# Kernel optimization log

Measured on AMD Instinct MI355X. Metric: run time of the kernel, lower is better.

The kernel has to match this reference:

```python
import jax, jax.numpy as jnp
import numpy as np

N, E, G = 50000, 800000, 64          # nodes, edges, graphs in batch
IN, H, F = 128, 4, 32                # in_dim, num_heads, out_feats per head
HD = H * F                           # 128 = flattened head dim
HID, OUT = 32, 10                    # hidden_dim, num classes
EPS, SLOPE = 1e-5, 0.2               # BN eps, leaky_relu negative slope


def batchnorm(x, g, b):
    mu = x.mean(0)
    var = x.var(0)  # biased, as torch BN in training mode
    return g * (x - mu) * jax.lax.rsqrt(var + EPS) + b


def gatv2(feat, src, dst, W, fb, attn, ob):
    # shared-weights GATv2: same fc for src and dst
    h = (feat @ W + fb).reshape(-1, H, F)           # [N,H,F]
    el = h[src]                                     # [E,H,F] gather
    er = h[dst]
    e = jnp.einsum('ehf,hf->eh', jax.nn.leaky_relu(el + er, SLOPE), attn)  # [E,H]
    # edge softmax over incoming edges of each dst node
    m = jax.ops.segment_max(e, dst, num_segments=N)
    m = jax.lax.stop_gradient(jnp.where(jnp.isfinite(m), m, 0.0))
    ex = jnp.exp(e - m[dst])
    den = jax.ops.segment_sum(ex, dst, num_segments=N)
    alpha = ex / jnp.where(den > 0, den, 1.0)[dst]  # zero in-degree -> zeros
    out = jax.ops.segment_sum((el * alpha[:, :, None]).reshape(-1, HD), dst,
                              num_segments=N)       # [N,HD]
    return jax.nn.relu(out + ob)                    # conv activation, flattened heads


def _forward(feat, src, dst, seg,
             w0, fb0, a0, ob0, bg0, bb0, lw0, lb0, lg0, lbt0,
             w1, fb1, a1, ob1, bg1, bb1, lw1, lb1, lg1, lbt1,
             w2, fb2, a2, ob2, bg2, bb2, lw2, lb2, lg2, lbt2,
             mw1, mg, mb, mw2):
    layers = [
        (w0, fb0, a0, ob0, bg0, bb0, lw0, lb0, lg0, lbt0),
        (w1, fb1, a1, ob1, bg1, bb1, lw1, lb1, lg1, lbt1),
        (w2, fb2, a2, ob2, bg2, bb2, lw2, lb2, lg2, lbt2),
    ]
    x = feat
    pooled = []
    for (W, fb, a, ob, bg, bb, lw, lb, lg, lbt) in layers:
        x = gatv2(x, src, dst, W, fb, a, ob)        # [N,HD]
        x = batchnorm(x, bg, bb)
        p = jax.ops.segment_sum(x, seg, num_segments=G)  # sum pool -> [G,HD]
        p = jax.nn.relu(p @ lw + lb)                # linear_prediction
        pooled.append(batchnorm(p, lg, lbt))        # [G,HID]
    ph = jnp.concatenate(pooled, axis=-1)           # [G, 3*HID]
    hmid = jax.nn.relu(batchnorm(ph @ mw1, mg, mb)) # MLP layer 1 (no bias)
    logits = hmid @ mw2                             # MLP layer 2 (no bias)
    return jax.nn.log_softmax(logits, axis=-1)      # [G,OUT]


def setup_inputs() -> dict:
    key = jax.random.key(0)
    ks = iter(jax.random.split(key, 64))
    d = {}
    d['feat'] = jax.random.normal(next(ks), (N, IN), dtype=jnp.float32)
    d['src'] = jax.random.randint(next(ks), (E,), 0, N, dtype=jnp.int32)
    d['dst'] = jax.random.randint(next(ks), (E,), 0, N, dtype=jnp.int32)
    d['seg'] = jnp.sort(jax.random.randint(next(ks), (N,), 0, G, dtype=jnp.int32))
    for i in range(3):
        d[f'w{i}'] = jax.random.normal(next(ks), (HD if i else IN, HD)) * 0.05
        d[f'fb{i}'] = jnp.zeros((HD,))
        d[f'a{i}'] = jax.random.normal(next(ks), (H, F)) * 0.05
        d[f'ob{i}'] = jnp.zeros((HD,))
        d[f'bg{i}'] = jnp.ones((HD,))
        d[f'bb{i}'] = jnp.zeros((HD,))
        d[f'lw{i}'] = jax.random.normal(next(ks), (HD, HID)) * 0.05
        d[f'lb{i}'] = jnp.zeros((HID,))
        d[f'lg{i}'] = jnp.ones((HID,))
        d[f'lbt{i}'] = jnp.zeros((HID,))
    d['mw1'] = jax.random.normal(next(ks), (3 * HID, HID)) * 0.05
    d['mg'] = jnp.ones((HID,))
    d['mb'] = jnp.zeros((HID,))
    d['mw2'] = jax.random.normal(next(ks), (HID, OUT)) * 0.05
    return d


def reference(feat, src, dst, seg,
              w0, fb0, a0, ob0, bg0, bb0, lw0, lb0, lg0, lbt0,
              w1, fb1, a1, ob1, bg1, bb1, lw1, lb1, lg1, lbt1,
              w2, fb2, a2, ob2, bg2, bb2, lw2, lb2, lg2, lbt2,
              mw1, mg, mb, mw2):
    return _forward(feat, src, dst, seg,
                    w0, fb0, a0, ob0, bg0, bb0, lw0, lb0, lg0, lbt0,
                    w1, fb1, a1, ob1, bg1, bb1, lw1, lb1, lg1, lbt1,
                    w2, fb2, a2, ob2, bg2, bb2, lw2, lb2, lg2, lbt2,
                    mw1, mg, mb, mw2)
```

## Files before the change

### kernel.cpp

```cpp
#include <hip/hip_runtime.h>
#include <math.h>

#define N_NODES 50000
#define N_EDGES 800000
#define G_GRAPHS 64
#define HDIM 128
#define HID 32
#define NCLS 10
#define BN_EPS 1e-5f
#define SLOPE 0.2f
#define NB_SCAN 196
#define STATS_STRIDE (256 + G_GRAPHS * HDIM)
#define DEFER_THR 8.0f

#define NBUCK 64
#define NPB 782
#define CH 4096
#define NCHUNK 196
#define NGB_GEMM 782
#define CAP_OUT 13824
#define NZ_DWORDS (64 + 3 * STATS_STRIDE + 64)

typedef __attribute__((ext_vector_type(8))) short bf16x8;
typedef __attribute__((ext_vector_type(4))) float f32x4;

__device__ __forceinline__ float lrelu(float x) { return fmaxf(x, SLOPE * x); }

__device__ __forceinline__ unsigned short f2bf(float x) {
    unsigned int u = __float_as_uint(x);
    u = (u + 0x7fffu + ((u >> 16) & 1u)) >> 16;
    return (unsigned short)u;
}
__device__ __forceinline__ unsigned int pk2bf(float lo, float hi) {
    unsigned int r;
    asm("v_cvt_pk_bf16_f32 %0, %1, %2" : "=v"(r) : "v"(lo), "v"(hi));
    return r;
}
__device__ __forceinline__ float2 up2(unsigned int u) {
    return make_float2(__uint_as_float(u << 16), __uint_as_float(u & 0xffff0000u));
}
__device__ __forceinline__ float bf2f(unsigned short u) {
    return __uint_as_float((unsigned int)u << 16);
}
__device__ __forceinline__ int wl_index(int k, int c) {
    int lane = ((k >> 3) & 3) * 16 + (c & 15);
    return (((k >> 5) * 8 + (c >> 4)) * 64 + lane) * 8 + (k & 7);
}

template <bool XF32>
__device__ __forceinline__ void gemm_body(int bid, const void* __restrict__ Xv,
                                          const unsigned short* __restrict__ WL,
                                          const float* __restrict__ fb,
                                          unsigned short* __restrict__ Hb) {
    int t = threadIdx.x;
    int w = t >> 6, lane = t & 63;
    int i16 = lane & 15, kg = lane >> 4;
    int r0w = bid * 64 + w * 16;
    int row = r0w + i16;
    int rowc = row < N_NODES ? row : N_NODES - 1;

    f32x4 acc[8];
    #pragma unroll
    for (int cs = 0; cs < 8; ++cs) acc[cs] = (f32x4){0.f, 0.f, 0.f, 0.f};

    #pragma unroll
    for (int ks = 0; ks < 4; ++ks) {
        union { uint4 u; bf16x8 s; } af;
        if (XF32) {
            const float* xp = (const float*)Xv + (size_t)rowc * HDIM + ks * 32 + kg * 8;
            float4 v0 = *(const float4*)xp;
            float4 v1 = *(const float4*)(xp + 4);
            af.u.x = pk2bf(v0.x, v0.y);
            af.u.y = pk2bf(v0.z, v0.w);
            af.u.z = pk2bf(v1.x, v1.y);
            af.u.w = pk2bf(v1.z, v1.w);
        } else {
            const unsigned short* xp = (const unsigned short*)Xv + (size_t)rowc * HDIM + ks * 32 + kg * 8;
            af.u = *(const uint4*)xp;
        }
        #pragma unroll
        for (int cs = 0; cs < 8; ++cs) {
            union { uint4 u; bf16x8 s; } bw;
            bw.u = *(const uint4*)&WL[(((ks << 3) + cs) * 64 + lane) * 8];
            acc[cs] = __builtin_amdgcn_mfma_f32_16x16x32_bf16(af.s, bw.s, acc[cs], 0, 0, 0);
        }
    }
    #pragma unroll
    for (int cs = 0; cs < 8; ++cs) {
        int col = cs * 16 + i16;
        float bias = fb[col];
        #pragma unroll
        for (int p = 0; p < 4; ++p) {
            int r = r0w + kg * 4 + p;
            if (r < N_NODES) Hb[(size_t)r * HDIM + col] = f2bf(acc[cs][p] + bias);
        }
    }
}

template <bool XF32>
__global__ __launch_bounds__(256) void k_gemm_mfma(const void* __restrict__ Xv,
                                                   const unsigned short* __restrict__ WL,
                                                   const float* __restrict__ fb,
                                                   unsigned short* __restrict__ Hb) {
    gemm_body<XF32>(blockIdx.x, Xv, WL, fb, Hb);
}

__global__ __launch_bounds__(256) void k_prep(const float* __restrict__ W,
                                              unsigned short* __restrict__ WL,
                                              unsigned int* __restrict__ zbase,
                                              const int* __restrict__ seg,
                                              int* __restrict__ gs) {
    int bid = blockIdx.x, t = threadIdx.x;
    if (bid < 16) {
        for (int idx = bid * 256 + t; idx < HDIM * HDIM; idx += 16 * 256) {
            int k = idx >> 7, c = idx & 127;
            WL[wl_index(k, c)] = f2bf(W[idx]);
        }
    } else if (bid < 20) {
        for (int i = (bid - 16) * 256 + t; i < NZ_DWORDS; i += 4 * 256) zbase[i] = 0u;
    } else {
        if (t <= G_GRAPHS) {
            int g = t;
            int lo = 0, hi = N_NODES;
            while (lo < hi) {
                int mid = (lo + hi) >> 1;
                if (seg[mid] < g) lo = mid + 1; else hi = mid;
            }
            gs[g] = lo;
        }
    }
}

__global__ __launch_bounds__(256) void k_mega0(const int* __restrict__ dst,
                                               int* __restrict__ bcnt,
                                               const unsigned short* __restrict__ WL0,
                                               const float* __restrict__ feat,
                                               const float* __restrict__ fb0,
                                               unsigned short* __restrict__ Hb) {
    __shared__ unsigned int h[NBUCK];
    int bid = blockIdx.x;
    int t = threadIdx.x;
    if (bid < NCHUNK) {
        if (t < NBUCK) h[t] = 0;
        __syncthreads();
        int base = bid * CH;
        #pragma unroll
        for (int e = 0; e < 16; ++e) {
            int i = base + e * 256 + t;
            if (i < N_EDGES) {
                int d = dst[i];
                atomicAdd(&h[d / NPB], 1u);
            }
        }
        __syncthreads();
        if (t < NBUCK && h[t]) atomicAdd(&bcnt[t], (int)h[t]);
    } else {
        gemm_body<true>(bid - NCHUNK, feat, WL0, fb0, Hb);
    }
}

__global__ __launch_bounds__(256) void k_bscatter(const int* __restrict__ dst,
                                                  const int* __restrict__ src,
                                                  const int* __restrict__ bcnt,
                                                  int* __restrict__ bcur,
                                                  unsigned int* __restrict__ gbuf) {
    __shared__ unsigned int hist[NBUCK];
    __shared__ unsigned int scanB[NBUCK + 1];
    __shared__ int gdelta[NBUCK];
    __shared__ unsigned int cur[NBUCK];
    __shared__ unsigned int ent[CH];
    __shared__ int bb[NBUCK];
    int t = threadIdx.x;
    int base = blockIdx.x * CH;
    unsigned int eb[16], een[16];
    if (t < NBUCK) {
        int v = bcnt[t];
        int inc = v;
        #pragma unroll
        for (int off = 1; off < 64; off <<= 1) {
            int u = __shfl_up(inc, off);
            if (t >= off) inc += u;
        }
        bb[t] = inc - v;
        hist[t] = 0;
    }
    __syncthreads();
    #pragma unroll
    for (int e = 0; e < 16; ++e) {
        int i = base + e * 256 + t;
        if (i < N_EDGES) {
            int d = dst[i];
            int s = src[i];
            int b = d / NPB;
            eb[e] = (unsigned int)b;
            een[e] = ((unsigned int)(d - b * NPB) << 17) | (unsigned int)s;
            atomicAdd(&hist[b], 1u);
        } else {
            eb[e] = 0xFFFFFFFFu;
            een[e] = 0;
        }
    }
    __syncthreads();
    if (t < NBUCK) {
        unsigned int v = hist[t];
        unsigned int inc = v;
        #pragma unroll
        for (int off = 1; off < 64; off <<= 1) {
            unsigned int u = __shfl_up(inc, off);
            if ((t & 63) >= off) inc += u;
        }
        scanB[t + 1] = inc;
        if (t == 0) scanB[0] = 0;
    }
    __syncthreads();
    if (t < NBUCK) {
        unsigned int hv = hist[t];
        int gb = bb[t] + (hv ? atomicAdd(&bcur[t], (int)hv) : 0);
        gdelta[t] = gb - (int)scanB[t];
        cur[t] = 0;
    }
    __syncthreads();
    #pragma unroll
    for (int e = 0; e < 16; ++e) {
        if (eb[e] < NBUCK) {
            unsigned int pos = scanB[eb[e]] + atomicAdd(&cur[eb[e]], 1u);
            ent[pos] = een[e];
        }
    }
    __syncthreads();
    unsigned int cntE = scanB[NBUCK];
    #pragma unroll
    for (int e = 0; e < 16; ++e) {
        unsigned int i = (unsigned int)(e * 256 + t);
        if (i < cntE) {
            int lo2 = 0, hi2 = NBUCK;
            while (hi2 - lo2 > 1) {
                int mid = (lo2 + hi2) >> 1;
                if (scanB[mid] <= i) lo2 = mid; else hi2 = mid;
            }
            gbuf[gdelta[lo2] + i] = ent[i];
        }
    }
}

__global__ __launch_bounds__(256) void k_bsort(const int* __restrict__ bcnt,
                                               const unsigned int* __restrict__ gbuf,
                                               int* __restrict__ ssrc,
                                               int* __restrict__ rowptr) {
    extern __shared__ unsigned int sout[];
    __shared__ unsigned int hist[NPB];
    __shared__ unsigned int sbase[NPB + 1];
    __shared__ unsigned int cur[NPB];
    __shared__ unsigned int wsum[4];
    __shared__ int sbb[NBUCK + 1];
    int b = blockIdx.x;
    int t = threadIdx.x;
    if (t < NBUCK) {
        int v = bcnt[t];
        int inc = v;
        #pragma unroll
        for (int off = 1; off < 64; off <<= 1) {
            int u = __shfl_up(inc, off);
            if (t >= off) inc += u;
        }
        sbb[t + 1] = inc;
        if (t == 0) sbb[0] = 0;
    }
    __syncthreads();
    int lo = sbb[b], hi = sbb[b + 1];
    int cnt = hi - lo;
    if (cnt > CAP_OUT) cnt = CAP_OUT;
    for (int i = t; i < NPB; i += 256) { hist[i] = 0; cur[i] = 0; }
    __syncthreads();
    for (int i = t; i < cnt; i += 256) {
        unsigned int e = gbuf[lo + i];
        atomicAdd(&hist[e >> 17], 1u);
    }
    __syncthreads();
    unsigned int loc[4], s = 0;
    #pragma unroll
    for (int j = 0; j < 4; ++j) {
        int idx = t * 4 + j;
        loc[j] = idx < NPB ? hist[idx] : 0;
        s += loc[j];
    }
    unsigned int inc = s;
    #pragma unroll
    for (int off = 1; off < 64; off <<= 1) {
        unsigned int u = __shfl_up(inc, off);
        if ((t & 63) >= off) inc += u;
    }
    int wid = t >> 6;
    if ((t & 63) == 63) wsum[wid] = inc;
    __syncthreads();
    if (t == 0) {
        unsigned int r = 0;
        #pragma unroll
        for (int w = 0; w < 4; ++w) { unsigned int x = wsum[w]; wsum[w] = r; r += x; }
    }
    __syncthreads();
    unsigned int excl = inc - s + wsum[wid];
    #pragma unroll
    for (int j = 0; j < 4; ++j) {
        int idx = t * 4 + j;
        if (idx < NPB) { sbase[idx] = excl; excl += loc[j]; }
    }
    if (t == 255) sbase[NPB] = excl;
    __syncthreads();
    for (int v = t; v < NPB; v += 256) {
        int nid = b * NPB + v;
        if (nid < N_NODES) rowptr[nid] = lo + (int)sbase[v];
    }
    if (b == NBUCK - 1 && t == 0) rowptr[N_NODES] = N_EDGES;
    for (int i = t; i < cnt; i += 256) {
        unsigned int e = gbuf[lo + i];
        unsigned int dl = e >> 17;
        unsigned int pos = sbase[dl] + atomicAdd(&cur[dl], 1u);
        if (pos < (unsigned int)CAP_OUT) sout[pos] = e & 0x1FFFFu;
    }
    __syncthreads();
    for (int i = t; i < cnt; i += 256) ssrc[lo + i] = (int)sout[i];
}

__global__ __launch_bounds__(256) void k_edge(const unsigned short* __restrict__ Hb,
                                              const int* __restrict__ row_ptr,
                                              const int* __restrict__ ssrc,
                                              const float* __restrict__ attn,
                                              const float* __restrict__ ob,
                                              unsigned short* __restrict__ Yb) {
    int wid = blockIdx.x * 4 + (threadIdx.x >> 6);
    if (wid >= N_NODES) return;
    int lane = threadIdx.x & 63;
    int slot = lane >> 4, s16 = lane & 15;
    int d0 = s16 << 3;
    int beg = row_ptr[wid], end = row_ptr[wid + 1];
    int deg = end - beg;
    if (deg == 0) {
        if (slot == 0) {
            float4 o0 = *(const float4*)&ob[d0];
            float4 o1 = *(const float4*)&ob[d0 + 4];
            uint4 w;
            w.x = pk2bf(fmaxf(o0.x, 0.f), fmaxf(o0.y, 0.f));
            w.y = pk2bf(fmaxf(o0.z, 0.f), fmaxf(o0.w, 0.f));
            w.z = pk2bf(fmaxf(o1.x, 0.f), fmaxf(o1.y, 0.f));
            w.w = pk2bf(fmaxf(o1.z, 0.f), fmaxf(o1.w, 0.f));
            *(uint4*)&Yb[(size_t)wid * HDIM + d0] = w;
        }
        return;
    }
    float er[8], at06[8], at04[8];
    {
        uint4 e = *(const uint4*)&Hb[(size_t)wid * HDIM + d0];
        unsigned int uu[4] = {e.x, e.y, e.z, e.w};
        #pragma unroll
        for (int i = 0; i < 4; ++i) {
            float2 f = up2(uu[i]);
            er[2 * i] = f.x; er[2 * i + 1] = f.y;
        }
        float4 a0 = *(const float4*)&attn[d0];
        float4 a1 = *(const float4*)&attn[d0 + 4];
        float av[8] = {a0.x, a0.y, a0.z, a0.w, a1.x, a1.y, a1.z, a1.w};
        #pragma unroll
        for (int d = 0; d < 8; ++d) {
            at06[d] = 0.6f * av[d];
            at04[d] = 0.4f * av[d];
        }
    }
    float cER = 0.f;
    #pragma unroll
    for (int d = 0; d < 8; ++d) cER = fmaf(at06[d], er[d], cER);
    cER += __shfl_xor(cER, 1);
    cER += __shfl_xor(cER, 2);

    const float NINF = __int_as_float(0xff800000);
    float m = -1e30f, den = 0.f;
    float acc[8] = {0.f, 0.f, 0.f, 0.f, 0.f, 0.f, 0.f, 0.f};
    int nit = (deg + 3) >> 2;
    int j = beg + slot;
    int sa;
    uint4 elc;
    {
        int jc0 = j < end ? j : beg;
        int jc1 = (j + 4) < end ? (j + 4) : beg;
        int s0 = ssrc[jc0];
        sa = ssrc[jc1];
        elc = *(const uint4*)&Hb[(size_t)s0 * HDIM + d0];
    }
    for (int it = 0; it < nit; ++it) {
        int jc2 = (j + 8) < end ? (j + 8) : beg;
        int sb = ssrc[jc2];
        uint4 eln = *(const uint4*)&Hb[(size_t)sa * HDIM + d0];
        bool act = j < end;
        float el[8];
        {
            unsigned int uu[4] = {elc.x, elc.y, elc.z, elc.w};
            #pragma unroll
            for (int i = 0; i < 4; ++i) {
                float2 f = up2(uu[i]);
                el[2 * i] = f.x; el[2 * i + 1] = f.y;
            }
        }
        float p = 0.f, pa = 0.f;
        #pragma unroll
        for (int d = 0; d < 8; ++d) {
            p = fmaf(at06[d], el[d], p);
            pa = fmaf(at04[d], fabsf(el[d] + er[d]), pa);
        }
        p += pa;
        p += __shfl_xor(p, 1);
        p += __shfl_xor(p, 2);
        float e = act ? (p + cER) : NINF;
        if (__all(e - m <= DEFER_THR)) {
            float q = __expf(e - m);
            den += q;
            #pragma unroll
            for (int d = 0; d < 8; ++d) acc[d] = fmaf(el[d], q, acc[d]);
        } else {
            float nm = fmaxf(m, e);
            float r = __expf(m - nm);
            float q = __expf(e - nm);
            den = fmaf(den, r, q);
            #pragma unroll
            for (int d = 0; d < 8; ++d) acc[d] = fmaf(acc[d], r, el[d] * q);
            m = nm;
        }
        elc = eln; sa = sb; j += 4;
    }
    #pragma unroll
    for (int st = 16; st <= 32; st <<= 1) {
        float m2 = __shfl_xor(m, st);
        float den2 = __shfl_xor(den, st);
        float nm = fmaxf(m, m2);
        float r1 = __expf(m - nm);
        float r2 = __expf(m2 - nm);
        den = den * r1 + den2 * r2;
        #pragma unroll
        for (int d = 0; d < 8; ++d) {
            float a2 = __shfl_xor(acc[d], st);
            acc[d] = acc[d] * r1 + a2 * r2;
        }
        m = nm;
    }
    if (slot == 0) {
        float inv = den > 0.f ? 1.f / den : 0.f;
        float4 o0 = *(const float4*)&ob[d0];
        float4 o1 = *(const float4*)&ob[d0 + 4];
        float o[8] = {o0.x, o0.y, o0.z, o0.w, o1.x, o1.y, o1.z, o1.w};
        float r[8];
        #pragma unroll
        for (int d = 0; d < 8; ++d) r[d] = fmaxf(fmaf(acc[d], inv, o[d]), 0.f);
        uint4 w;
        w.x = pk2bf(r[0], r[1]);
        w.y = pk2bf(r[2], r[3]);
        w.z = pk2bf(r[4], r[5]);
        w.w = pk2bf(r[6], r[7]);
        *(uint4*)&Yb[(size_t)wid * HDIM + d0] = w;
    }
}

__global__ __launch_bounds__(256) void k_stats_pool(const unsigned short* __restrict__ Yb,
                                                    const int* __restrict__ seg,
                                                    float* __restrict__ sums,
                                                    float* __restrict__ sumsq,
                                                    float* __restrict__ pooled) {
    __shared__ float4 red[256];
    __shared__ int sseg[256];
    int t = threadIdx.x;
    int r0 = blockIdx.x * 256;
    if (r0 + t < N_NODES) sseg[t] = seg[r0 + t];
    __syncthreads();
    int c4 = t & 31, rh = t >> 5;
    int rend = r0 + 256 < N_NODES ? r0 + 256 : N_NODES;
    float sx = 0.f, sy = 0.f, sz = 0.f, sw = 0.f;
    float qx = 0.f, qy = 0.f, qz = 0.f, qw = 0.f;
    int curg = -1;
    float rx = 0.f, ry = 0.f, rz = 0.f, rw = 0.f;
    for (int r = r0 + rh; r < rend; r += 8) {
        ushort4 v = *(const ushort4*)&Yb[(size_t)r * HDIM + c4 * 4];
        float x0 = bf2f(v.x), x1 = bf2f(v.y), x2 = bf2f(v.z), x3 = bf2f(v.w);
        sx += x0; sy += x1; sz += x2; sw += x3;
        qx = fmaf(x0, x0, qx); qy = fmaf(x1, x1, qy);
        qz = fmaf(x2, x2, qz); qw = fmaf(x3, x3, qw);
        int g = sseg[r - r0];
        if (g != curg) {
            if (curg >= 0) {
                float* pp = &pooled[curg * HDIM + c4 * 4];
                atomicAdd(pp + 0, rx); atomicAdd(pp + 1, ry);
                atomicAdd(pp + 2, rz); atomicAdd(pp + 3, rw);
            }
            curg = g;
            rx = x0; ry = x1; rz = x2; rw = x3;
        } else {
            rx += x0; ry += x1; rz += x2; rw += x3;
        }
    }
    if (curg >= 0) {
        float* pp = &pooled[curg * HDIM + c4 * 4];
        atomicAdd(pp + 0, rx); atomicAdd(pp + 1, ry);
        atomicAdd(pp + 2, rz); atomicAdd(pp + 3, rw);
    }
    red[t] = make_float4(sx, sy, sz, sw);
    __syncthreads();
    if (rh == 0) {
        float4 tot = red[c4];
        #pragma unroll
        for (int i = 1; i < 8; ++i) {
            float4 o = red[i * 32 + c4];
            tot.x += o.x; tot.y += o.y; tot.z += o.z; tot.w += o.w;
        }
        float* sp = &sums[c4 * 4];
        atomicAdd(sp + 0, tot.x); atomicAdd(sp + 1, tot.y);
        atomicAdd(sp + 2, tot.z); atomicAdd(sp + 3, tot.w);
    }
    __syncthreads();
    red[t] = make_float4(qx, qy, qz, qw);
    __syncthreads();
    if (rh == 0) {
        float4 tot = red[c4];
        #pragma unroll
        for (int i = 1; i < 8; ++i) {
            float4 o = red[i * 32 + c4];
            tot.x += o.x; tot.y += o.y; tot.z += o.z; tot.w += o.w;
        }
        float* sp = &sumsq[c4 * 4];
        atomicAdd(sp + 0, tot.x); atomicAdd(sp + 1, tot.y);
        atomicAdd(sp + 2, tot.z); atomicAdd(sp + 3, tot.w);
    }
}

__global__ __launch_bounds__(256) void k_fold(const float* __restrict__ sums,
                                              const float* __restrict__ sumsq,
                                              const float* __restrict__ bng,
                                              const float* __restrict__ bnb,
                                              const float* __restrict__ Wnext,
                                              const float* __restrict__ fbnext,
                                              unsigned short* __restrict__ WLnext,
                                              float* __restrict__ Fbnext) {
    __shared__ float sA[HDIM], sB[HDIM];
    int t = threadIdx.x;
    if (t < HDIM) {
        float mu = sums[t] * (1.f / N_NODES);
        float var = fmaxf(sumsq[t] * (1.f / N_NODES) - mu * mu, 0.f);
        float inv = rsqrtf(var + BN_EPS);
        float a = bng[t] * inv;
        sA[t] = a;
        sB[t] = bnb[t] - a * mu;
    }
    __syncthreads();
    if (blockIdx.x < 64) {
        int idx = blockIdx.x * 256 + t;
        int k = idx >> 7, c = idx & 127;
        WLnext[wl_index(k, c)] = f2bf(sA[k] * Wnext[idx]);
    } else if (t < HDIM) {
        float a = fbnext[t];
        for (int k = 0; k < HDIM; ++k) a = fmaf(sB[k], Wnext[k * HDIM + t], a);
        Fbnext[t] = a;
    }
}

__global__ __launch_bounds__(256) void k_heads1(const float* __restrict__ statsAll,
                                                const int* __restrict__ gs,
                                                const float* __restrict__ bng0, const float* __restrict__ bnb0,
                                                const float* __restrict__ bng1, const float* __restrict__ bnb1,
                                                const float* __restrict__ bng2, const float* __restrict__ bnb2,
                                                const float* __restrict__ lw0, const float* __restrict__ lb0,
                                                const float* __restrict__ lw1, const float* __restrict__ lb1,
                                                const float* __restrict__ lw2, const float* __restrict__ lb2,
                                                float* __restrict__ pl_all) {
    __shared__ float sA3[3][HDIM], sB3[3][HDIM];
    __shared__ float red[8][HID];
    int g = blockIdx.x, t = threadIdx.x;
    const float* bngs[3] = {bng0, bng1, bng2};
    const float* bnbs[3] = {bnb0, bnb1, bnb2};
    const float* lws[3] = {lw0, lw1, lw2};
    const float* lbs[3] = {lb0, lb1, lb2};
    if (t < HDIM) {
        #pragma unroll
        for (int l = 0; l < 3; ++l) {
            const float* su = statsAll + (size_t)l * STATS_STRIDE;
            float mu = su[t] * (1.f / N_NODES);
            float var = fmaxf(su[128 + t] * (1.f / N_NODES) - mu * mu, 0.f);
            float inv = rsqrtf(var + BN_EPS);
            float a = bngs[l][t] * inv;
            sA3[l][t] = a;
            sB3[l][t] = bnbs[l][t] - a * mu;
        }
    }
    __syncthreads();
    float cnt = (float)(gs[g + 1] - gs[g]);
    int col = t & 31, kq = t >> 5;
    #pragma unroll
    for (int l = 0; l < 3; ++l) {
        const float* pg = statsAll + (size_t)l * STATS_STRIDE + 256 + (size_t)g * HDIM;
        float part = 0.f;
        #pragma unroll
        for (int kk = 0; kk < 16; ++kk) {
            int k = kq * 16 + kk;
            float pin = fmaf(sA3[l][k], pg[k], cnt * sB3[l][k]);
            part = fmaf(pin, lws[l][k * HID + col], part);
        }
        red[kq][col] = part;
        __syncthreads();
        if (kq == 0) {
            float s = red[0][col] + red[1][col] + red[2][col] + red[3][col]
                    + red[4][col] + red[5][col] + red[6][col] + red[7][col];
            pl_all[((size_t)l * G_GRAPHS + g) * HID + col] = fmaxf(s + lbs[l][col], 0.f);
        }
        __syncthreads();
    }
}

__global__ __launch_bounds__(256) void k_final(const float* __restrict__ pl_all,
                                               const float* __restrict__ lg0, const float* __restrict__ lbt0,
                                               const float* __restrict__ lg1, const float* __restrict__ lbt1,
                                               const float* __restrict__ lg2, const float* __restrict__ lbt2,
                                               const float* __restrict__ mw1,
                                               const float* __restrict__ mg,
                                               const float* __restrict__ mb,
                                               const float* __restrict__ mw2,
                                               float* __restrict__ out) {
    __shared__ float pl3[3 * G_GRAPHS * HID];
    __shared__ float w1[3 * HID * HID];
    __shared__ float hm[G_GRAPHS][HID];
    __shared__ float sc[96], sh[96];
    __shared__ float lgt[G_GRAPHS][NCLS];
    __shared__ float w2[HID * NCLS];
    int t = threadIdx.x;
    const float* lgs[3] = {lg0, lg1, lg2};
    const float* lbts[3] = {lbt0, lbt1, lbt2};
    for (int i = t; i < 3 * G_GRAPHS * HID; i += 256) pl3[i] = pl_all[i];
    for (int i = t; i < 3 * HID * HID; i += 256) w1[i] = mw1[i];
    for (int i = t; i < HID * NCLS; i += 256) w2[i] = mw2[i];
    __syncthreads();
    if (t < 96) {
        int l = t >> 5, c = t & 31;
        float s = 0.f, q = 0.f;
        for (int g = 0; g < G_GRAPHS; ++g) {
            float v = pl3[(l * G_GRAPHS + g) * HID + c];
            s += v; q = fmaf(v, v, q);
        }
        float mu = s * (1.f / G_GRAPHS);
        float var = fmaxf(q * (1.f / G_GRAPHS) - mu * mu, 0.f);
        float inv = rsqrtf(var + BN_EPS);
        float a = lgs[l][c] * inv;
        sc[t] = a;
        sh[t] = lbts[l][c] - a * mu;
    }
    __syncthreads();
    for (int i = t; i < 3 * G_GRAPHS * HID; i += 256) {
        int l = i / (G_GRAPHS * HID);
        int c = i & 31;
        pl3[i] = fmaf(pl3[i], sc[l * 32 + c], sh[l * 32 + c]);
    }
    __syncthreads();
    for (int i = t; i < G_GRAPHS * HID; i += 256) {
        int g = i >> 5, c = i & 31;
        float acc = 0.f;
        #pragma unroll
        for (int l = 0; l < 3; ++l)
            for (int k = 0; k < HID; ++k)
                acc = fmaf(pl3[(l * G_GRAPHS + g) * HID + k], w1[(l * HID + k) * HID + c], acc);
        hm[g][c] = acc;
    }
    __syncthreads();
    if (t < HID) {
        float s = 0.f, q = 0.f;
        for (int g = 0; g < G_GRAPHS; ++g) {
            float v = hm[g][t];
            s += v; q = fmaf(v, v, q);
        }
        float mu = s * (1.f / G_GRAPHS);
        float var = fmaxf(q * (1.f / G_GRAPHS) - mu * mu, 0.f);
        float inv = rsqrtf(var + BN_EPS);
        float a = mg[t] * inv;
        sc[t] = a;
        sh[t] = mb[t] - a * mu;
    }
    __syncthreads();
    for (int i = t; i < G_GRAPHS * HID; i += 256) {
        int g = i >> 5, c = i & 31;
        hm[g][c] = fmaxf(fmaf(hm[g][c], sc[c], sh[c]), 0.f);
    }
    __syncthreads();
    for (int i = t; i < G_GRAPHS * NCLS; i += 256) {
        int g = i / NCLS, c = i % NCLS;
        float acc = 0.f;
        for (int k = 0; k < HID; ++k) acc = fmaf(hm[g][k], w2[k * NCLS + c], acc);
        lgt[g][c] = acc;
    }
    __syncthreads();
    if (t < G_GRAPHS) {
        float mx = -INFINITY;
        for (int c = 0; c < NCLS; ++c) mx = fmaxf(mx, lgt[t][c]);
        float s = 0.f;
        for (int c = 0; c < NCLS; ++c) s += expf(lgt[t][c] - mx);
        float lse = mx + logf(s);
        for (int c = 0; c < NCLS; ++c) out[t * NCLS + c] = lgt[t][c] - lse;
    }
}

extern "C" void kernel_launch(void* const* d_in, const int* in_sizes, int n_in,
                              void* d_out, int out_size, void* d_ws, size_t ws_size,
                              hipStream_t stream) {
    (void)in_sizes; (void)n_in; (void)out_size; (void)ws_size;
    const float* feat = (const float*)d_in[0];
    const int* src = (const int*)d_in[1];
    const int* dst = (const int*)d_in[2];
    const int* seg = (const int*)d_in[3];
    auto LP = [&](int l, int j) { return (const float*)d_in[4 + 10 * l + j]; };
    const float* mw1 = (const float*)d_in[34];
    const float* mg  = (const float*)d_in[35];
    const float* mb  = (const float*)d_in[36];
    const float* mw2 = (const float*)d_in[37];

    char* p = (char*)d_ws;
    auto alloc = [&](size_t bytes) { char* r = p; p += (bytes + 255) & ~(size_t)255; return r; };
    unsigned short* Hb = (unsigned short*)alloc((size_t)N_NODES * HDIM * 2);
    unsigned short* Yb = (unsigned short*)alloc((size_t)N_NODES * HDIM * 2);
    int*   ssrc   = (int*)alloc((size_t)N_EDGES * 4);
    unsigned int* gbuf = (unsigned int*)alloc((size_t)N_EDGES * 4);
    int*   rp     = (int*)alloc((size_t)(N_NODES + 1) * 4);
    int*   bcnt   = (int*)alloc((size_t)NBUCK * 4);
    float* statsAll = (float*)alloc((size_t)3 * STATS_STRIDE * 4);
    int*   bcur   = (int*)alloc((size_t)NBUCK * 4);
    float* pl_all = (float*)alloc((size_t)3 * G_GRAPHS * HID * 4);
    int*   gs     = (int*)alloc((size_t)(G_GRAPHS + 1) * 4);
    unsigned short* WL = (unsigned short*)alloc((size_t)3 * HDIM * HDIM * 2);
    float* Fb     = (float*)alloc((size_t)3 * HDIM * 4);

    k_prep<<<21, 256, 0, stream>>>(LP(0, 0), WL, (unsigned int*)bcnt, seg, gs);
    k_mega0<<<NCHUNK + NGB_GEMM, 256, 0, stream>>>(dst, bcnt, WL, feat, LP(0, 1), Hb);
    k_bscatter<<<NCHUNK, 256, 0, stream>>>(dst, src, bcnt, bcur, gbuf);
    k_bsort<<<NBUCK, 256, CAP_OUT * 4, stream>>>(bcnt, gbuf, ssrc, rp);

    for (int l = 0; l < 3; ++l) {
        float* sums   = statsAll + (size_t)l * STATS_STRIDE;
        float* sumsq  = sums + 128;
        float* pooled = sums + 256;
        if (l > 0) {
            k_gemm_mfma<false><<<NGB_GEMM, 256, 0, stream>>>(
                Yb, WL + (size_t)l * HDIM * HDIM, Fb + (size_t)l * HDIM, Hb);
        }
        k_edge<<<(N_NODES + 3) / 4, 256, 0, stream>>>(Hb, rp, ssrc, LP(l, 2), LP(l, 3), Yb);
        k_stats_pool<<<NB_SCAN, 256, 0, stream>>>(Yb, seg, sums, sumsq, pooled);
        if (l < 2) {
            k_fold<<<65, 256, 0, stream>>>(sums, sumsq, LP(l, 4), LP(l, 5),
                                           LP(l + 1, 0), LP(l + 1, 1),
                                           WL + (size_t)(l + 1) * HDIM * HDIM,
                                           Fb + (size_t)(l + 1) * HDIM);
        }
    }
    k_heads1<<<G_GRAPHS, 256, 0, stream>>>(statsAll, gs,
                                           LP(0, 4), LP(0, 5), LP(1, 4), LP(1, 5), LP(2, 4), LP(2, 5),
                                           LP(0, 6), LP(0, 7), LP(1, 6), LP(1, 7), LP(2, 6), LP(2, 7),
                                           pl_all);
    k_final<<<1, 256, 0, stream>>>(pl_all,
                                   LP(0, 8), LP(0, 9), LP(1, 8), LP(1, 9), LP(2, 8), LP(2, 9),
                                   mw1, mg, mb, mw2, (float*)d_out);
}
```

Before: 362.5 us.

## Fuse BN fold into stats kernel and heads into final via last-block counters

The separate k_fold launch is merged into the stats/pool kernel, and k_heads1 is merged with k_final. In each case the last block to finish, found through an atomic counter, does the serial tail work, which removes three kernel launches and their gaps. The edge kernel also goes back to a direct leaky-relu attention score instead of the split 0.6/0.4 abs formulation with a precomputed dst term. That costs some extra ALU per edge but needs fewer registers. The counters rely on workspace zeroing, which is presumably widened through NZ_DWORDS, and the last-block pattern depends on threadfence ordering.

New measurement: 358.7 us. No clear change (-1.1%).

```diff
diff --git a/kernel.cpp b/kernel.cpp
--- a/kernel.cpp
+++ b/kernel.cpp
@@ -19,7 +19,7 @@
 #define NCHUNK 196
 #define NGB_GEMM 782
 #define CAP_OUT 13824
-#define NZ_DWORDS (64 + 3 * STATS_STRIDE + 64)
+#define NZ_DWORDS (64 + 3 * STATS_STRIDE + 64 + 64)
 
 typedef __attribute__((ext_vector_type(8))) short bf16x8;
 typedef __attribute__((ext_vector_type(4))) float f32x4;
@@ -348,7 +348,7 @@
         }
         return;
     }
-    float er[8], at06[8], at04[8];
+    float er[8], at[8];
     {
         uint4 e = *(const uint4*)&Hb[(size_t)wid * HDIM + d0];
         unsigned int uu[4] = {e.x, e.y, e.z, e.w};
@@ -359,19 +359,9 @@
         }
         float4 a0 = *(const float4*)&attn[d0];
         float4 a1 = *(const float4*)&attn[d0 + 4];
-        float av[8] = {a0.x, a0.y, a0.z, a0.w, a1.x, a1.y, a1.z, a1.w};
-        #pragma unroll
-        for (int d = 0; d < 8; ++d) {
-            at06[d] = 0.6f * av[d];
-            at04[d] = 0.4f * av[d];
-        }
-    }
-    float cER = 0.f;
-    #pragma unroll
-    for (int d = 0; d < 8; ++d) cER = fmaf(at06[d], er[d], cER);
-    cER += __shfl_xor(cER, 1);
-    cER += __shfl_xor(cER, 2);
-
+        at[0] = a0.x; at[1] = a0.y; at[2] = a0.z; at[3] = a0.w;
+        at[4] = a1.x; at[5] = a1.y; at[6] = a1.z; at[7] = a1.w;
+    }
     const float NINF = __int_as_float(0xff800000);
     float m = -1e30f, den = 0.f;
     float acc[8] = {0.f, 0.f, 0.f, 0.f, 0.f, 0.f, 0.f, 0.f};
@@ -400,16 +390,12 @@
                 el[2 * i] = f.x; el[2 * i + 1] = f.y;
             }
         }
-        float p = 0.f, pa = 0.f;
-        #pragma unroll
-        for (int d = 0; d < 8; ++d) {
-            p = fmaf(at06[d], el[d], p);
-            pa = fmaf(at04[d], fabsf(el[d] + er[d]), pa);
-        }
-        p += pa;
+        float p = 0.f;
+        #pragma unroll
+        for (int d = 0; d < 8; ++d) p = fmaf(lrelu(el[d] + er[d]), at[d], p);
         p += __shfl_xor(p, 1);
         p += __shfl_xor(p, 2);
-        float e = act ? (p + cER) : NINF;
+        float e = act ? p : NINF;
         if (__all(e - m <= DEFER_THR)) {
             float q = __expf(e - m);
             den += q;
@@ -458,13 +444,22 @@
     }
 }
 
-__global__ __launch_bounds__(256) void k_stats_pool(const unsigned short* __restrict__ Yb,
+__global__ __launch_bounds__(256) void k_stats_fold(const unsigned short* __restrict__ Yb,
                                                     const int* __restrict__ seg,
                                                     float* __restrict__ sums,
                                                     float* __restrict__ sumsq,
-                                                    float* __restrict__ pooled) {
+                                                    float* __restrict__ pooled,
+                                                    const float* __restrict__ bng,
+                                                    const float* __restrict__ bnb,
+                                                    const float* __restrict__ Wnext,
+                                                    const float* __restrict__ fbnext,
+                                                    unsigned short* __restrict__ WLnext,
+                                                    float* __restrict__ Fbnext,
+                                                    int* __restrict__ counter) {
     __shared__ float4 red[256];
     __shared__ int sseg[256];
+    __shared__ float sA[HDIM], sB[HDIM];
+    __shared__ unsigned int lastFlag;
     int t = threadIdx.x;
     int r0 = blockIdx.x * 256;
     if (r0 + t < N_NODES) sseg[t] = seg[r0 + t];
@@ -526,49 +521,55 @@
         atomicAdd(sp + 0, tot.x); atomicAdd(sp + 1, tot.y);
         atomicAdd(sp + 2, tot.z); atomicAdd(sp + 3, tot.w);
     }
-}
-
-__global__ __launch_bounds__(256) void k_fold(const float* __restrict__ sums,
-                                              const float* __restrict__ sumsq,
-                                              const float* __restrict__ bng,
-                                              const float* __restrict__ bnb,
-                                              const float* __restrict__ Wnext,
-                                              const float* __restrict__ fbnext,
-                                              unsigned short* __restrict__ WLnext,
-                                              float* __restrict__ Fbnext) {
-    __shared__ float sA[HDIM], sB[HDIM];
-    int t = threadIdx.x;
+    if (!Wnext) return;
+    __threadfence();
+    if (t == 0) lastFlag = (atomicAdd(counter, 1) == NB_SCAN - 1) ? 1u : 0u;
+    __syncthreads();
+    if (!lastFlag) return;
+    __threadfence();
     if (t < HDIM) {
-        float mu = sums[t] * (1.f / N_NODES);
-        float var = fmaxf(sumsq[t] * (1.f / N_NODES) - mu * mu, 0.f);
+        float sv = atomicAdd(&sums[t], 0.f);
+        float qv = atomicAdd(&sumsq[t], 0.f);
+        float mu = sv * (1.f / N_NODES);
+        float var = fmaxf(qv * (1.f / N_NODES) - mu * mu, 0.f);
         float inv = rsqrtf(var + BN_EPS);
         float a = bng[t] * inv;
         sA[t] = a;
         sB[t] = bnb[t] - a * mu;
     }
     __syncthreads();
-    if (blockIdx.x < 64) {
-        int idx = blockIdx.x * 256 + t;
+    for (int idx = t; idx < HDIM * HDIM; idx += 256) {
         int k = idx >> 7, c = idx & 127;
         WLnext[wl_index(k, c)] = f2bf(sA[k] * Wnext[idx]);
-    } else if (t < HDIM) {
+    }
+    if (t < HDIM) {
         float a = fbnext[t];
         for (int k = 0; k < HDIM; ++k) a = fmaf(sB[k], Wnext[k * HDIM + t], a);
         Fbnext[t] = a;
     }
 }
 
-__global__ __launch_bounds__(256) void k_heads1(const float* __restrict__ statsAll,
-                                                const int* __restrict__ gs,
-                                                const float* __restrict__ bng0, const float* __restrict__ bnb0,
-                                                const float* __restrict__ bng1, const float* __restrict__ bnb1,
-                                                const float* __restrict__ bng2, const float* __restrict__ bnb2,
-                                                const float* __restrict__ lw0, const float* __restrict__ lb0,
-                                                const float* __restrict__ lw1, const float* __restrict__ lb1,
-                                                const float* __restrict__ lw2, const float* __restrict__ lb2,
-                                                float* __restrict__ pl_all) {
+__global__ __launch_bounds__(256) void k_headsfinal(const float* __restrict__ statsAll,
+                                                    const int* __restrict__ gs,
+                                                    const float* __restrict__ bng0, const float* __restrict__ bnb0,
+                                                    const float* __restrict__ bng1, const float* __restrict__ bnb1,
+                                                    const float* __restrict__ bng2, const float* __restrict__ bnb2,
+                                                    const float* __restrict__ lw0, const float* __restrict__ lb0,
+                                                    const float* __restrict__ lw1, const float* __restrict__ lb1,
+                                                    const float* __restrict__ lw2, const float* __restrict__ lb2,
+                                                    float* __restrict__ pl_all,
+                                                    const float* __restrict__ lg0, const float* __restrict__ lbt0,
+                                                    const float* __restrict__ lg1, const float* __restrict__ lbt1,
+                                                    const float* __restrict__ lg2, const float* __restrict__ lbt2,
+                                                    const float* __restrict__ mw1,
+                                                    const float* __restrict__ mg,
+                                                    const float* __restrict__ mb,
+                                                    const float* __restrict__ mw2,
+                                                    float* __restrict__ out,
+                                                    int* __restrict__ counter) {
     __shared__ float sA3[3][HDIM], sB3[3][HDIM];
     __shared__ float red[8][HID];
+    __shared__ unsigned int lastFlag;
     int g = blockIdx.x, t = threadIdx.x;
     const float* bngs[3] = {bng0, bng1, bng2};
     const float* bnbs[3] = {bnb0, bnb1, bnb2};
@@ -587,7 +588,7 @@
         }
     }
     __syncthreads();
-    float cnt = (float)(gs[g + 1] - gs[g]);
+    float cntg = (float)(gs[g + 1] - gs[g]);
     int col = t & 31, kq = t >> 5;
     #pragma unroll
     for (int l = 0; l < 3; ++l) {
@@ -596,7 +597,7 @@
         #pragma unroll
         for (int kk = 0; kk < 16; ++kk) {
             int k = kq * 16 + kk;
-            float pin = fmaf(sA3[l][k], pg[k], cnt * sB3[l][k]);
+            float pin = fmaf(sA3[l][k], pg[k], cntg * sB3[l][k]);
             part = fmaf(pin, lws[l][k * HID + col], part);
         }
         red[kq][col] = part;
@@ -608,94 +609,89 @@
         }
         __syncthreads();
     }
-}
-
-__global__ __launch_bounds__(256) void k_final(const float* __restrict__ pl_all,
-                                               const float* __restrict__ lg0, const float* __restrict__ lbt0,
-                                               const float* __restrict__ lg1, const float* __restrict__ lbt1,
-                                               const float* __restrict__ lg2, const float* __restrict__ lbt2,
-                                               const float* __restrict__ mw1,
-                                               const float* __restrict__ mg,
-                                               const float* __restrict__ mb,
-                                               const float* __restrict__ mw2,
-                                               float* __restrict__ out) {
-    __shared__ float pl3[3 * G_GRAPHS * HID];
-    __shared__ float w1[3 * HID * HID];
-    __shared__ float hm[G_GRAPHS][HID];
-    __shared__ float sc[96], sh[96];
-    __shared__ float lgt[G_GRAPHS][NCLS];
-    __shared__ float w2[HID * NCLS];
-    int t = threadIdx.x;
-    const float* lgs[3] = {lg0, lg1, lg2};
-    const float* lbts[3] = {lbt0, lbt1, lbt2};
-    for (int i = t; i < 3 * G_GRAPHS * HID; i += 256) pl3[i] = pl_all[i];
-    for (int i = t; i < 3 * HID * HID; i += 256) w1[i] = mw1[i];
-    for (int i = t; i < HID * NCLS; i += 256) w2[i] = mw2[i];
-    __syncthreads();
-    if (t < 96) {
-        int l = t >> 5, c = t & 31;
-        float s = 0.f, q = 0.f;
-        for (int g = 0; g < G_GRAPHS; ++g) {
-            float v = pl3[(l * G_GRAPHS + g) * HID + c];
-            s += v; q = fmaf(v, v, q);
-        }
-        float mu = s * (1.f / G_GRAPHS);
-        float var = fmaxf(q * (1.f / G_GRAPHS) - mu * mu, 0.f);
-        float inv = rsqrtf(var + BN_EPS);
-        float a = lgs[l][c] * inv;
-        sc[t] = a;
-        sh[t] = lbts[l][c] - a * mu;
-    }
-    __syncthreads();
-    for (int i = t; i < 3 * G_GRAPHS * HID; i += 256) {
-        int l = i / (G_GRAPHS * HID);
-        int c = i & 31;
-        pl3[i] = fmaf(pl3[i], sc[l * 32 + c], sh[l * 32 + c]);
-    }
-    __syncthreads();
-    for (int i = t; i < G_GRAPHS * HID; i += 256) {
-        int g = i >> 5, c = i & 31;
-        float acc = 0.f;
-        #pragma unroll
-        for (int l = 0; l < 3; ++l)
-            for (int k = 0; k < HID; ++k)
-                acc = fmaf(pl3[(l * G_GRAPHS + g) * HID + k], w1[(l * HID + k) * HID + c], acc);
-        hm[g][c] = acc;
-    }
-    __syncthreads();
-    if (t < HID) {
-        float s = 0.f, q = 0.f;
-        for (int g = 0; g < G_GRAPHS; ++g) {
-            float v = hm[g][t];
-            s += v; q = fmaf(v, v, q);
-        }
-        float mu = s * (1.f / G_GRAPHS);
-        float var = fmaxf(q * (1.f / G_GRAPHS) - mu * mu, 0.f);
-        float inv = rsqrtf(var + BN_EPS);
-        float a = mg[t] * inv;
-        sc[t] = a;
-        sh[t] = mb[t] - a * mu;
-    }
-    __syncthreads();
-    for (int i = t; i < G_GRAPHS * HID; i += 256) {
-        int g = i >> 5, c = i & 31;
-        hm[g][c] = fmaxf(fmaf(hm[g][c], sc[c], sh[c]), 0.f);
-    }
-    __syncthreads();
-    for (int i = t; i < G_GRAPHS * NCLS; i += 256) {
-        int g = i / NCLS, c = i % NCLS;
-        float acc = 0.f;
-        for (int k = 0; k < HID; ++k) acc = fmaf(hm[g][k], w2[k * NCLS + c], acc);
-        lgt[g][c] = acc;
-    }
-    __syncthreads();
-    if (t < G_GRAPHS) {
-        float mx = -INFINITY;
-        for (int c = 0; c < NCLS; ++c) mx = fmaxf(mx, lgt[t][c]);
-        float s = 0.f;
-        for (int c = 0; c < NCLS; ++c) s += expf(lgt[t][c] - mx);
-        float lse = mx + logf(s);
-        for (int c = 0; c < NCLS; ++c) out[t * NCLS + c] = lgt[t][c] - lse;
+    __threadfence();
+    if (t == 0) lastFlag = (atomicAdd(counter, 1) == G_GRAPHS - 1) ? 1u : 0u;
+    __syncthreads();
+    if (!lastFlag) return;
+    __threadfence();
+    {
+        __shared__ float pl3[3 * G_GRAPHS * HID];
+        __shared__ float w1[3 * HID * HID];
+        __shared__ float hm[G_GRAPHS][HID];
+        __shared__ float sc[96], sh[96];
+        __shared__ float lgt[G_GRAPHS][NCLS];
+        __shared__ float w2[HID * NCLS];
+        const float* lgs[3] = {lg0, lg1, lg2};
+        const float* lbts[3] = {lbt0, lbt1, lbt2};
+        for (int i = t; i < 3 * G_GRAPHS * HID; i += 256) pl3[i] = pl_all[i];
+        for (int i = t; i < 3 * HID * HID; i += 256) w1[i] = mw1[i];
+        for (int i = t; i < HID * NCLS; i += 256) w2[i] = mw2[i];
+        __syncthreads();
+        if (t < 96) {
+            int l = t >> 5, c = t & 31;
+            float s = 0.f, q = 0.f;
+            for (int gg = 0; gg < G_GRAPHS; ++gg) {
+                float v = pl3[(l * G_GRAPHS + gg) * HID + c];
+                s += v; q = fmaf(v, v, q);
+            }
+            float mu = s * (1.f / G_GRAPHS);
+            float var = fmaxf(q * (1.f / G_GRAPHS) - mu * mu, 0.f);
+            float inv = rsqrtf(var + BN_EPS);
+            float a = lgs[l][c] * inv;
+            sc[t] = a;
+            sh[t] = lbts[l][c] - a * mu;
+        }
+        __syncthreads();
+        for (int i = t; i < 3 * G_GRAPHS * HID; i += 256) {
+            int l = i / (G_GRAPHS * HID);
+            int c = i & 31;
+            pl3[i] = fmaf(pl3[i], sc[l * 32 + c], sh[l * 32 + c]);
+        }
+        __syncthreads();
+        for (int i = t; i < G_GRAPHS * HID; i += 256) {
+            int gg = i >> 5, c = i & 31;
+            float acc = 0.f;
+            #pragma unroll
+            for (int l = 0; l < 3; ++l)
+                for (int k = 0; k < HID; ++k)
+                    acc = fmaf(pl3[(l * G_GRAPHS + gg) * HID + k], w1[(l * HID + k) * HID + c], acc);
+            hm[gg][c] = acc;
+        }
+        __syncthreads();
+        if (t < HID) {
+            float s = 0.f, q = 0.f;
+            for (int gg = 0; gg < G_GRAPHS; ++gg) {
+                float v = hm[gg][t];
+                s += v; q = fmaf(v, v, q);
+            }
+            float mu = s * (1.f / G_GRAPHS);
+            float var = fmaxf(q * (1.f / G_GRAPHS) - mu * mu, 0.f);
+            float inv = rsqrtf(var + BN_EPS);
+            float a = mg[t] * inv;
+            sc[t] = a;
+            sh[t] = mb[t] - a * mu;
+        }
+        __syncthreads();
+        for (int i = t; i < G_GRAPHS * HID; i += 256) {
+            int gg = i >> 5, c = i & 31;
+            hm[gg][c] = fmaxf(fmaf(hm[gg][c], sc[c], sh[c]), 0.f);
+        }
+        __syncthreads();
+        for (int i = t; i < G_GRAPHS * NCLS; i += 256) {
+            int gg = i / NCLS, c = i % NCLS;
+            float acc = 0.f;
+            for (int k = 0; k < HID; ++k) acc = fmaf(hm[gg][k], w2[k * NCLS + c], acc);
+            lgt[gg][c] = acc;
+        }
+        __syncthreads();
+        if (t < G_GRAPHS) {
+            float mx = -INFINITY;
+            for (int c = 0; c < NCLS; ++c) mx = fmaxf(mx, lgt[t][c]);
+            float s = 0.f;
+            for (int c = 0; c < NCLS; ++c) s += expf(lgt[t][c] - mx);
+            float lse = mx + logf(s);
+            for (int c = 0; c < NCLS; ++c) out[t * NCLS + c] = lgt[t][c] - lse;
+        }
     }
 }
 
@@ -723,6 +719,7 @@
     int*   bcnt   = (int*)alloc((size_t)NBUCK * 4);
     float* statsAll = (float*)alloc((size_t)3 * STATS_STRIDE * 4);
     int*   bcur   = (int*)alloc((size_t)NBUCK * 4);
+    int*   cnts   = (int*)alloc((size_t)64 * 4);
     float* pl_all = (float*)alloc((size_t)3 * G_GRAPHS * HID * 4);
     int*   gs     = (int*)alloc((size_t)(G_GRAPHS + 1) * 4);
     unsigned short* WL = (unsigned short*)alloc((size_t)3 * HDIM * HDIM * 2);
@@ -742,19 +739,19 @@
                 Yb, WL + (size_t)l * HDIM * HDIM, Fb + (size_t)l * HDIM, Hb);
         }
         k_edge<<<(N_NODES + 3) / 4, 256, 0, stream>>>(Hb, rp, ssrc, LP(l, 2), LP(l, 3), Yb);
-        k_stats_pool<<<NB_SCAN, 256, 0, stream>>>(Yb, seg, sums, sumsq, pooled);
-        if (l < 2) {
-            k_fold<<<65, 256, 0, stream>>>(sums, sumsq, LP(l, 4), LP(l, 5),
-                                           LP(l + 1, 0), LP(l + 1, 1),
-                                           WL + (size_t)(l + 1) * HDIM * HDIM,
-                                           Fb + (size_t)(l + 1) * HDIM);
-        }
-    }
-    k_heads1<<<G_GRAPHS, 256, 0, stream>>>(statsAll, gs,
-                                           LP(0, 4), LP(0, 5), LP(1, 4), LP(1, 5), LP(2, 4), LP(2, 5),
-                                           LP(0, 6), LP(0, 7), LP(1, 6), LP(1, 7), LP(2, 6), LP(2, 7),
-                                           pl_all);
-    k_final<<<1, 256, 0, stream>>>(pl_all,
-                                   LP(0, 8), LP(0, 9), LP(1, 8), LP(1, 9), LP(2, 8), LP(2, 9),
-                                   mw1, mg, mb, mw2, (float*)d_out);
-}
+        int isLast = (l == 2);
+        k_stats_fold<<<NB_SCAN, 256, 0, stream>>>(
+            Yb, seg, sums, sumsq, pooled, LP(l, 4), LP(l, 5),
+            isLast ? nullptr : LP(l + 1, 0), isLast ? nullptr : LP(l + 1, 1),
+            isLast ? nullptr : WL + (size_t)(l + 1) * HDIM * HDIM,
+            isLast ? nullptr : Fb + (size_t)(l + 1) * HDIM,
+            cnts + l);
+    }
+    k_headsfinal<<<G_GRAPHS, 256, 0, stream>>>(
+        statsAll, gs,
+        LP(0, 4), LP(0, 5), LP(1, 4), LP(1, 5), LP(2, 4), LP(2, 5),
+        LP(0, 6), LP(0, 7), LP(1, 6), LP(1, 7), LP(2, 6), LP(2, 7),
+        pl_all,
+        LP(0, 8), LP(0, 9), LP(1, 8), LP(1, 9), LP(2, 8), LP(2, 9),
+        mw1, mg, mb, mw2, (float*)d_out, cnts + 3);
+}
```
